# Optimization experiments

Measured on AMD Instinct MI355X. Metric: run time of the kernel, lower is better.

Reference implementation:

```python
import jax, jax.numpy as jnp
import numpy as np

N_NODES = 100000
N_EDGES = 1200000
MAX_ATOM_TYPE = 100
NUM_FEATURES = 92
GC_DIM = 64          # pre_layer_dim == gc_dim == CGConv channels
NUM_RBF = 32
NUM_GC_LAYERS = 4
CUTOFF_UPPER = 5.0
BN_EPS = 1e-5


def setup_inputs() -> dict:
    key = jax.random.key(0)
    ks = jax.random.split(key, 12)
    atom_types = jax.random.randint(ks[0], (N_NODES,), 0, MAX_ATOM_TYPE, dtype=jnp.int32)
    pos = jax.random.uniform(ks[1], (N_NODES, 3), dtype=jnp.float32) * 6.0  # box side 6 -> many dists < cutoff
    edge_index = jax.random.randint(ks[2], (2, N_EDGES), 0, N_NODES, dtype=jnp.int32)
    # parameters
    emb = jax.random.normal(ks[3], (MAX_ATOM_TYPE, NUM_FEATURES), dtype=jnp.float32)
    s = 1.0 / np.sqrt(NUM_FEATURES)
    pre_W = jax.random.uniform(ks[4], (NUM_FEATURES, GC_DIM), minval=-s, maxval=s, dtype=jnp.float32)
    pre_b = jnp.zeros((GC_DIM,), jnp.float32)
    zdim = 2 * GC_DIM + NUM_RBF  # [x_i, x_j, edge_attr]
    sz = 1.0 / np.sqrt(zdim)
    Wf = jax.random.uniform(ks[5], (NUM_GC_LAYERS, zdim, GC_DIM), minval=-sz, maxval=sz, dtype=jnp.float32)
    bf = jnp.zeros((NUM_GC_LAYERS, GC_DIM), jnp.float32)
    Ws = jax.random.uniform(ks[6], (NUM_GC_LAYERS, zdim, GC_DIM), minval=-sz, maxval=sz, dtype=jnp.float32)
    bs = jnp.zeros((NUM_GC_LAYERS, GC_DIM), jnp.float32)
    bn_gamma = jnp.ones((NUM_GC_LAYERS, GC_DIM), jnp.float32)
    bn_beta = jnp.zeros((NUM_GC_LAYERS, GC_DIM), jnp.float32)
    # ExpNormalSmearing (torchmd-net) init
    start = np.exp(-CUTOFF_UPPER)
    means = jnp.asarray(np.linspace(start, 1.0, NUM_RBF), jnp.float32)
    betas = jnp.full((NUM_RBF,), (2.0 / NUM_RBF * (1.0 - start)) ** -2, jnp.float32)
    return {"atom_types": atom_types, "pos": pos, "edge_index": edge_index,
            "emb": emb, "pre_W": pre_W, "pre_b": pre_b,
            "Wf": Wf, "bf": bf, "Ws": Ws, "bs": bs,
            "bn_gamma": bn_gamma, "bn_beta": bn_beta,
            "means": means, "betas": betas}


def _forward(atom_types, pos, edge_index, emb, pre_W, pre_b, Wf, bf, Ws, bs,
             bn_gamma, bn_beta, means, betas):
    src, dst = edge_index[0], edge_index[1]
    # distance (edge_vec = pos[src] - pos[dst])
    vec = pos[src] - pos[dst]                                  # [E,3]
    dist = jnp.sqrt(jnp.sum(vec * vec, axis=-1) + 1e-12)       # [E]
    # expnorm RBF with cosine cutoff (cutoff_lower = 0)
    cutoff = 0.5 * (jnp.cos(dist * (np.pi / CUTOFF_UPPER)) + 1.0) * (dist < CUTOFF_UPPER)
    alpha = 5.0 / CUTOFF_UPPER
    edge_attr = cutoff[:, None] * jnp.exp(
        -betas * (jnp.exp(-alpha * dist)[:, None] - means) ** 2)  # [E,NUM_RBF]
    # embedding + pre layer
    x = emb[atom_types]                                        # [N,F]
    x = jax.nn.relu(x @ pre_W + pre_b)                         # [N,C]
    # mean-aggregation degree (scatter-mean denominator)
    deg = jax.ops.segment_sum(jnp.ones_like(dist), dst, num_segments=N_NODES)
    inv_deg = jnp.where(deg > 0, 1.0 / jnp.maximum(deg, 1.0), 0.0)[:, None]
    for l in range(NUM_GC_LAYERS):
        # CGConv: z = [x_i, x_j, e]; out = x + mean_j(sigmoid(lin_f(z)) * softplus(lin_s(z)))
        z = jnp.concatenate([x[dst], x[src], edge_attr], axis=-1)   # [E, 2C+R]
        msg = jax.nn.sigmoid(z @ Wf[l] + bf[l]) * jax.nn.softplus(z @ Ws[l] + bs[l])
        agg = jax.ops.segment_sum(msg, dst, num_segments=N_NODES) * inv_deg
        x = x + agg
        # BatchNorm1d (batch statistics, biased var, as in torch training mode)
        mu = jnp.mean(x, axis=0)
        var = jnp.mean((x - mu) ** 2, axis=0)
        x = (x - mu) * jax.lax.rsqrt(var + BN_EPS) * bn_gamma[l] + bn_beta[l]
    return x


def reference(atom_types, pos, edge_index, emb, pre_W, pre_b, Wf, bf, Ws, bs,
              bn_gamma, bn_beta, means, betas):
    return _forward(atom_types, pos, edge_index, emb, pre_W, pre_b, Wf, bf, Ws, bs,
                    bn_gamma, bn_beta, means, betas)
```

## Files before the change

kernel.cpp:

```cpp
#include <hip/hip_runtime.h>
#include <math.h>

#define N_NODES 100000
#define N_EDGES 1200000
#define GC 64
#define RBF 32
#define NLAYERS 4
#define NF 92
#define NATOM 100
#define BN_EPS 1e-5f
#define TILE_GRID 2048
#define NWIN (N_EDGES / 16)
#define LOG2E 1.44269504f
#define LN2 0.69314718f

typedef _Float16 half8 __attribute__((ext_vector_type(8)));
typedef _Float16 half4 __attribute__((ext_vector_type(4)));
typedef _Float16 half2v __attribute__((ext_vector_type(2)));
typedef float f32x4 __attribute__((ext_vector_type(4)));
union U32H2 { unsigned int u; half2v h; };

__global__ __launch_bounds__(256) void deg_kernel(
    const int* __restrict__ ei, int* __restrict__ deg)
{
    int e = blockIdx.x * 256 + threadIdx.x;
    if (e >= N_EDGES) return;
    atomicAdd(&deg[ei[N_EDGES + e]], 1);
}

__global__ __launch_bounds__(256) void scan_a_kernel(const int* __restrict__ deg, int* __restrict__ bsums)
{
    __shared__ int sm[256];
    int tid = threadIdx.x;
    int i = blockIdx.x * 256 + tid;
    int v = (i < N_NODES) ? deg[i] : 0;
    sm[tid] = v;
    __syncthreads();
    for (int s = 128; s > 0; s >>= 1) {
        if (tid < s) sm[tid] += sm[tid + s];
        __syncthreads();
    }
    if (tid == 0) bsums[blockIdx.x] = sm[0];
}

__global__ __launch_bounds__(512) void scan_b_kernel(const int* __restrict__ bsums, int* __restrict__ boffs)
{
    __shared__ int sm[512];
    int tid = threadIdx.x;
    int v = (tid < 391) ? bsums[tid] : 0;
    sm[tid] = v;
    __syncthreads();
    for (int off = 1; off < 512; off <<= 1) {
        int t = (tid >= off) ? sm[tid - off] : 0;
        __syncthreads();
        sm[tid] += t;
        __syncthreads();
    }
    boffs[tid] = (tid == 0) ? 0 : sm[tid - 1];
}

__global__ __launch_bounds__(256) void scan_c_kernel(
    const int* __restrict__ deg, const int* __restrict__ boffs,
    int* __restrict__ row_st, float* __restrict__ inv_deg)
{
    __shared__ int sm[256];
    int tid = threadIdx.x;
    int i = blockIdx.x * 256 + tid;
    int v = (i < N_NODES) ? deg[i] : 0;
    sm[tid] = v;
    __syncthreads();
    for (int off = 1; off < 256; off <<= 1) {
        int t = (tid >= off) ? sm[tid - off] : 0;
        __syncthreads();
        sm[tid] += t;
        __syncthreads();
    }
    if (i <= N_NODES) row_st[i] = boffs[blockIdx.x] + sm[tid] - v;
    if (i < N_NODES) inv_deg[i] = (v > 0) ? (1.0f / (float)v) : 0.0f;
}

__global__ __launch_bounds__(256) void scatter_perm_kernel(
    const int* __restrict__ ei, const int* __restrict__ row_st,
    int* __restrict__ cursor, int* __restrict__ csr_src, int* __restrict__ csr_dst)
{
    int e = blockIdx.x * 256 + threadIdx.x;
    if (e >= N_EDGES) return;
    int s = ei[e];
    int d = ei[N_EDGES + e];
    int p = atomicAdd(&cursor[d], 1);
    int idx = row_st[d] + p;
    csr_src[idx] = s;
    csr_dst[idx] = d;
}

__global__ __launch_bounds__(256) void rbf_kernel(
    const int* __restrict__ csr_src, const int* __restrict__ csr_dst,
    const float* __restrict__ pos,
    const float* __restrict__ means, const float* __restrict__ betas,
    unsigned int* __restrict__ ea)
{
    int idx = blockIdx.x * 256 + threadIdx.x;
    if (idx >= N_EDGES) return;
    int s = csr_src[idx];
    int d = csr_dst[idx];
    float dx = pos[s * 3 + 0] - pos[d * 3 + 0];
    float dy = pos[s * 3 + 1] - pos[d * 3 + 1];
    float dz = pos[s * 3 + 2] - pos[d * 3 + 2];
    float dist = sqrtf(dx * dx + dy * dy + dz * dz + 1e-12f);

    float cut = 0.0f;
    if (dist < 5.0f) cut = 0.5f * (__cosf(dist * 0.6283185307179586f) + 1.0f);
    float ex = __expf(-dist);
    union { _Float16 h[32]; uint4 u[4]; } pk;
#pragma unroll
    for (int k = 0; k < 32; k++) {
        float v = ex - means[k];
        pk.h[k] = (_Float16)(cut * __expf(-betas[k] * v * v));
    }
    uint4* op = (uint4*)(ea + (size_t)idx * 16);
    op[0] = pk.u[0];
    op[1] = pk.u[1];
    op[2] = pk.u[2];
    op[3] = pk.u[3];
}

__global__ __launch_bounds__(256) void window_prep_kernel(
    const int* __restrict__ csr_dst, const float* __restrict__ inv_deg,
    unsigned char* __restrict__ seg8, int* __restrict__ wnode, _Float16* __restrict__ inv_e)
{
    int w = blockIdx.x * 256 + threadIdx.x;
    if (w >= NWIN) return;
    int base = w * 16;
    int prev = -1, s = -1;
    for (int k = 0; k < 16; k++) {
        int d = csr_dst[base + k];
        if (d != prev) { s++; prev = d; wnode[base + s] = d; }
        seg8[base + k] = (unsigned char)s;
        inv_e[base + k] = (_Float16)(inv_deg[d] * LN2);
    }
    for (int m = s + 1; m < 16; m++) wnode[base + m] = -1;
}

__global__ __launch_bounds__(256) void wcvt_kernel(
    const float* __restrict__ Wf, const float* __restrict__ Ws,
    _Float16* __restrict__ wf16, _Float16* __restrict__ ws16)
{
    int i = blockIdx.x * 256 + threadIdx.x;
    int l = i / (160 * GC);
    int r = i - l * 160 * GC;
    int k = r >> 6;
    int col = r & 63;
    size_t o = ((size_t)l * GC + col) * 160 + k;
    wf16[o] = (_Float16)(Wf[i] * LOG2E);
    ws16[o] = (_Float16)(Ws[i] * LOG2E);
}

__global__ __launch_bounds__(64) void atom_table_kernel(
    const float* __restrict__ emb, const float* __restrict__ pre_W,
    const float* __restrict__ pre_b, float* __restrict__ T)
{
    int a = blockIdx.x;
    int c = threadIdx.x;
    float acc = pre_b[c];
    for (int k = 0; k < NF; k++) acc = fmaf(emb[a * NF + k], pre_W[k * GC + c], acc);
    T[a * GC + c] = fmaxf(acc, 0.0f);
}

__global__ __launch_bounds__(256) void xinit_kernel(
    const int* __restrict__ atom_types, const float* __restrict__ T,
    float* __restrict__ x, _Float16* __restrict__ x16)
{
    int i = blockIdx.x * 256 + threadIdx.x;
    int n = i >> 4;
    int a = atom_types[n];
    float4 v = ((const float4*)T)[a * 16 + (i & 15)];
    ((float4*)x)[i] = v;
    half4 h = { (_Float16)v.x, (_Float16)v.y, (_Float16)v.z, (_Float16)v.w };
    ((half4*)x16)[i] = h;
}

static __device__ __forceinline__ void proj_mfma16(
    const _Float16* __restrict__ wf, const _Float16* __restrict__ ws,
    const float* __restrict__ bfv, const float* __restrict__ bsv,
    const half8 Bn[2], int cb, int node, unsigned int* __restrict__ P2u)
{
    const int lane = threadIdx.x & 63;
    const int quad = lane >> 4;
    const int r16 = lane & 15;
    f32x4 accf[2], accs[2];
#pragma unroll
    for (int sub = 0; sub < 2; sub++) {
        accf[sub] = (f32x4){0.f, 0.f, 0.f, 0.f};
        accs[sub] = (f32x4){0.f, 0.f, 0.f, 0.f};
    }
#pragma unroll
    for (int kt = 0; kt < 2; kt++) {
#pragma unroll
        for (int sub = 0; sub < 2; sub++) {
            int chan = cb + sub * 16 + r16;
            half8 a = *(const half8*)(wf + (size_t)chan * 160 + kt * 32 + quad * 8);
            half8 b = *(const half8*)(ws + (size_t)chan * 160 + kt * 32 + quad * 8);
            accf[sub] = __builtin_amdgcn_mfma_f32_16x16x32_f16(a, Bn[kt], accf[sub], 0, 0, 0);
            accs[sub] = __builtin_amdgcn_mfma_f32_16x16x32_f16(b, Bn[kt], accs[sub], 0, 0, 0);
        }
    }
#pragma unroll
    for (int sub = 0; sub < 2; sub++) {
        float4 bf4 = *(const float4*)(bfv + cb + sub * 16 + quad * 4);
        float4 bs4 = *(const float4*)(bsv + cb + sub * 16 + quad * 4);
        half8 h = { (_Float16)(accf[sub][0] + bf4.x * LOG2E), (_Float16)(accs[sub][0] + bs4.x * LOG2E),
                    (_Float16)(accf[sub][1] + bf4.y * LOG2E), (_Float16)(accs[sub][1] + bs4.y * LOG2E),
                    (_Float16)(accf[sub][2] + bf4.z * LOG2E), (_Float16)(accs[sub][2] + bs4.z * LOG2E),
                    (_Float16)(accf[sub][3] + bf4.w * LOG2E), (_Float16)(accs[sub][3] + bs4.w * LOG2E) };
        *(half8*)(P2u + (size_t)node * GC + cb + sub * 16 + quad * 4) = h;
    }
}

__global__ __launch_bounds__(256) void proj_kernel(
    const _Float16* __restrict__ x16,
    const _Float16* __restrict__ wf, const _Float16* __restrict__ ws,
    const float* __restrict__ bfv, const float* __restrict__ bsv,
    unsigned int* __restrict__ P2u)
{
    const int lane = threadIdx.x & 63;
    const int wid = threadIdx.x >> 6;
    const int quad = lane >> 4;
    const int r16 = lane & 15;
    const int wgid = blockIdx.x * 4 + wid;
    const int cb = (wgid & 1) * 32;
    const int nb = (wgid >> 1) * 16;
    half8 Bn[2];
    Bn[0] = *(const half8*)(x16 + (size_t)(nb + r16) * GC + quad * 8);
    Bn[1] = *(const half8*)(x16 + (size_t)(nb + r16) * GC + 32 + quad * 8);
    proj_mfma16(wf, ws, bfv, bsv, Bn, cb, nb + r16, P2u);
}

__global__ __launch_bounds__(256) void bnproj_kernel(
    const float* __restrict__ xn, const float* __restrict__ stats,
    const float* __restrict__ gamma, const float* __restrict__ beta,
    float* __restrict__ xout, _Float16* __restrict__ x16,
    const _Float16* __restrict__ wf, const _Float16* __restrict__ ws,
    const float* __restrict__ bfv, const float* __restrict__ bsv,
    unsigned int* __restrict__ P2u)
{
    __shared__ _Float16 lx[32 * 72];
    const int nb = blockIdx.x * 32;
    const float invN = 1.0f / (float)N_NODES;

#pragma unroll
    for (int rep = 0; rep < 2; rep++) {
        int g = rep * 256 + threadIdx.x;
        int gi = blockIdx.x * 512 + g;
        int node = g >> 4;
        int c4 = (g & 15) * 4;
        float4 v = ((const float4*)xn)[gi];
        float vv[4] = {v.x, v.y, v.z, v.w};
        float o[4];
#pragma unroll
        for (int t = 0; t < 4; t++) {
            int c = c4 + t;
            float mu = stats[c] * invN;
            float var = stats[64 + c] * invN - mu * mu;
            float sc = gamma[c] * rsqrtf(var + BN_EPS);
            o[t] = (vv[t] - mu) * sc + beta[c];
        }
        ((float4*)xout)[gi] = make_float4(o[0], o[1], o[2], o[3]);
        half4 h = { (_Float16)o[0], (_Float16)o[1], (_Float16)o[2], (_Float16)o[3] };
        ((half4*)x16)[gi] = h;
        *(half4*)(lx + node * 72 + c4) = h;
    }
    __syncthreads();

    const int lane = threadIdx.x & 63;
    const int wid = threadIdx.x >> 6;
    const int quad = lane >> 4;
    const int r16 = lane & 15;
    const int cb = (wid & 1) * 32;
    const int tn = (wid >> 1) * 16 + r16;
    half8 Bn[2];
    Bn[0] = *(const half8*)(lx + tn * 72 + quad * 8);
    Bn[1] = *(const half8*)(lx + tn * 72 + 32 + quad * 8);
    proj_mfma16(wf, ws, bfv, bsv, Bn, cb, nb + tn, P2u);
}

static __device__ __forceinline__ void compute_win(
    half8 S0, half8 S1, half8 E,
    const unsigned int (&pv)[8], unsigned int segq, int4 wn4, half4 inv4,
    const half8 (&WGF)[3][2], const half8 (&WGS)[3][2],
    int r16, int quad, int cb, float* __restrict__ x)
{
    f32x4 accf[2], accs[2];
#pragma unroll
    for (int ctl = 0; ctl < 2; ctl++) {
#pragma unroll
        for (int rr = 0; rr < 4; rr++) {
            U32H2 t; t.u = pv[ctl * 4 + rr];
            accf[ctl][rr] = (float)t.h.x;
            accs[ctl][rr] = (float)t.h.y;
        }
    }
    __builtin_amdgcn_s_setprio(1);
#pragma unroll
    for (int ctl = 0; ctl < 2; ctl++) {
        accf[ctl] = __builtin_amdgcn_mfma_f32_16x16x32_f16(S0, WGF[0][ctl], accf[ctl], 0, 0, 0);
        accs[ctl] = __builtin_amdgcn_mfma_f32_16x16x32_f16(S0, WGS[0][ctl], accs[ctl], 0, 0, 0);
        accf[ctl] = __builtin_amdgcn_mfma_f32_16x16x32_f16(S1, WGF[1][ctl], accf[ctl], 0, 0, 0);
        accs[ctl] = __builtin_amdgcn_mfma_f32_16x16x32_f16(S1, WGS[1][ctl], accs[ctl], 0, 0, 0);
        accf[ctl] = __builtin_amdgcn_mfma_f32_16x16x32_f16(E,  WGF[2][ctl], accf[ctl], 0, 0, 0);
        accs[ctl] = __builtin_amdgcn_mfma_f32_16x16x32_f16(E,  WGS[2][ctl], accs[ctl], 0, 0, 0);
    }
    __builtin_amdgcn_s_setprio(0);
    half4 msgh[2];
#pragma unroll
    for (int ctl = 0; ctl < 2; ctl++) {
#pragma unroll
        for (int rr = 0; rr < 4; rr++) {
            float af = accf[ctl][rr];
            float as = accs[ctl][rr];
            float sg = __builtin_amdgcn_rcpf(1.0f + __builtin_amdgcn_exp2f(-af));
            float sp = __builtin_amdgcn_logf(1.0f + __builtin_amdgcn_exp2f(as));
            msgh[ctl][rr] = (_Float16)(sg * sp);
        }
    }
    half4 am;
#pragma unroll
    for (int j = 0; j < 4; j++) {
        int sj = (segq >> (8 * j)) & 0xff;
        am[j] = (sj == r16) ? inv4[j] : (_Float16)0.0f;
    }
    int wa[4] = { wn4.x, wn4.y, wn4.z, wn4.w };
    const f32x4 zf = (f32x4){0.0f, 0.0f, 0.0f, 0.0f};
#pragma unroll
    for (int ctl = 0; ctl < 2; ctl++) {
        f32x4 red = __builtin_amdgcn_mfma_f32_16x16x16f16(am, msgh[ctl], zf, 0, 0, 0);
#pragma unroll
        for (int rr = 0; rr < 4; rr++) {
            int nd = wa[rr];
            if (nd >= 0) atomicAdd(&x[(size_t)nd * GC + cb + ctl * 16 + r16], red[rr]);
        }
    }
}

#define LOADSET(S0_, S1_, EE_, SGQ_, WN4_, INV4_, PV_, SRC_, D4_, WW_)               \
    S0_ = *(const half8*)(x16 + (size_t)(SRC_) * GC + quad * 8);                     \
    S1_ = *(const half8*)(x16 + (size_t)(SRC_) * GC + 32 + quad * 8);                \
    EE_ = *(const half8*)(ea + ((size_t)(WW_) * 16 + r16) * RBF + quad * 8);         \
    SGQ_ = *(const unsigned int*)(seg8 + (WW_) * 16 + quad * 4);                     \
    WN4_ = *(const int4*)(wnode + (WW_) * 16 + quad * 4);                            \
    INV4_ = *(const half4*)(inv_e + (WW_) * 16 + quad * 4);                          \
    {                                                                                 \
        int dd0 = (D4_).x, dd1 = (D4_).y, dd2 = (D4_).z, dd3 = (D4_).w;              \
        PV_[0] = P2u[(size_t)dd0 * GC + cb + r16];                                   \
        PV_[1] = P2u[(size_t)dd1 * GC + cb + r16];                                   \
        PV_[2] = P2u[(size_t)dd2 * GC + cb + r16];                                   \
        PV_[3] = P2u[(size_t)dd3 * GC + cb + r16];                                   \
        PV_[4] = P2u[(size_t)dd0 * GC + cb + 16 + r16];                              \
        PV_[5] = P2u[(size_t)dd1 * GC + cb + 16 + r16];                              \
        PV_[6] = P2u[(size_t)dd2 * GC + cb + 16 + r16];                              \
        PV_[7] = P2u[(size_t)dd3 * GC + cb + 16 + r16];                              \
    }

__global__ __launch_bounds__(256, 3) void win_mfma_kernel(
    const _Float16* __restrict__ x16, const _Float16* __restrict__ ea,
    const int* __restrict__ csr_src, const int* __restrict__ csr_dst,
    const unsigned char* __restrict__ seg8, const int* __restrict__ wnode,
    const _Float16* __restrict__ inv_e, const unsigned int* __restrict__ P2u,
    const _Float16* __restrict__ wf16, const _Float16* __restrict__ ws16,
    float* __restrict__ x)
{
    const int lane = threadIdx.x & 63;
    const int wid = __builtin_amdgcn_readfirstlane(threadIdx.x >> 6);
    const int quad = lane >> 4;
    const int r16 = lane & 15;
    const int wgid = blockIdx.x * 4 + wid;
    const int cb = (wgid & 1) * 32;
    int w = wgid >> 1;
    const int NSEQ = TILE_GRID * 2;

    half8 WGF[3][2], WGS[3][2];
#pragma unroll
    for (int ctl = 0; ctl < 2; ctl++) {
        const _Float16* wfp = wf16 + (size_t)(cb + ctl * 16 + r16) * 160 + 64 + quad * 8;
        const _Float16* wsp = ws16 + (size_t)(cb + ctl * 16 + r16) * 160 + 64 + quad * 8;
#pragma unroll
        for (int kt = 0; kt < 3; kt++) {
            WGF[kt][ctl] = *(const half8*)(wfp + kt * 32);
            WGS[kt][ctl] = *(const half8*)(wsp + kt * 32);
        }
    }

    int sA = csr_src[w * 16 + r16];
    int4 d4A = *(const int4*)(csr_dst + w * 16 + quad * 4);
    half8 AS0, AS1, AE;
    unsigned int apv[8], asgq;
    int4 awn4;
    half4 ainv4;
    LOADSET(AS0, AS1, AE, asgq, awn4, ainv4, apv, sA, d4A, w);

    int wB = w + NSEQ; if (wB >= NWIN) wB = NWIN - 1;
    int sB = csr_src[wB * 16 + r16];
    int4 d4B = *(const int4*)(csr_dst + wB * 16 + quad * 4);
    half8 BS0, BS1, BE;
    unsigned int bpv[8], bsgq;
    int4 bwn4;
    half4 binv4;
    LOADSET(BS0, BS1, BE, bsgq, bwn4, binv4, bpv, sB, d4B, wB);

    int wC = wB + NSEQ; if (wC >= NWIN) wC = NWIN - 1;
    int sC = csr_src[wC * 16 + r16];
    int4 d4C = *(const int4*)(csr_dst + wC * 16 + quad * 4);

    while (true) {
        compute_win(AS0, AS1, AE, apv, asgq, awn4, ainv4,
                    WGF, WGS, r16, quad, cb, x);
        LOADSET(AS0, AS1, AE, asgq, awn4, ainv4, apv, sC, d4C, wC);
        wC += NSEQ; if (wC >= NWIN) wC = NWIN - 1;
        sC = csr_src[wC * 16 + r16];
        d4C = *(const int4*)(csr_dst + wC * 16 + quad * 4);
        w += NSEQ;
        if (w >= NWIN) break;

        compute_win(BS0, BS1, BE, bpv, bsgq, bwn4, binv4,
                    WGF, WGS, r16, quad, cb, x);
        LOADSET(BS0, BS1, BE, bsgq, bwn4, binv4, bpv, sC, d4C, wC);
        wC += NSEQ; if (wC >= NWIN) wC = NWIN - 1;
        sC = csr_src[wC * 16 + r16];
        d4C = *(const int4*)(csr_dst + wC * 16 + quad * 4);
        w += NSEQ;
        if (w >= NWIN) break;
    }
}

__global__ __launch_bounds__(256) void stats_kernel(const float* __restrict__ x, float* __restrict__ stats)
{
    const int lane = threadIdx.x & 63;
    const int wid = threadIdx.x >> 6;
    int w = blockIdx.x * 4 + wid;
    float s1 = 0.0f, s2 = 0.0f;
    for (int n = w; n < N_NODES; n += 1024) {
        float v = x[(size_t)n * GC + lane];
        s1 += v;
        s2 = fmaf(v, v, s2);
    }
    __shared__ float rs1[4][64];
    __shared__ float rs2[4][64];
    rs1[wid][lane] = s1;
    rs2[wid][lane] = s2;
    __syncthreads();
    if (threadIdx.x < 64) {
        atomicAdd(&stats[lane], rs1[0][lane] + rs1[1][lane] + rs1[2][lane] + rs1[3][lane]);
    } else if (threadIdx.x < 128) {
        int c = threadIdx.x & 63;
        atomicAdd(&stats[64 + c], rs2[0][c] + rs2[1][c] + rs2[2][c] + rs2[3][c]);
    }
}

__global__ __launch_bounds__(256) void bn_kernel(
    const float* __restrict__ xn, const float* __restrict__ stats,
    const float* __restrict__ gamma, const float* __restrict__ beta,
    float* __restrict__ out)
{
    int i = blockIdx.x * 256 + threadIdx.x;
    int c4 = (i & 15) * 4;
    float4 v = ((const float4*)xn)[i];
    float vv[4] = {v.x, v.y, v.z, v.w};
    float o[4];
    const float invN = 1.0f / (float)N_NODES;
#pragma unroll
    for (int t = 0; t < 4; t++) {
        int c = c4 + t;
        float mu = stats[c] * invN;
        float var = stats[64 + c] * invN - mu * mu;
        float sc = gamma[c] * rsqrtf(var + BN_EPS);
        o[t] = (vv[t] - mu) * sc + beta[c];
    }
    ((float4*)out)[i] = make_float4(o[0], o[1], o[2], o[3]);
}

extern "C" void kernel_launch(void* const* d_in, const int* in_sizes, int n_in,
                              void* d_out, int out_size, void* d_ws, size_t ws_size,
                              hipStream_t stream)
{
    const int* atom_types = (const int*)d_in[0];
    const float* pos = (const float*)d_in[1];
    const int* edge_index = (const int*)d_in[2];
    const float* emb = (const float*)d_in[3];
    const float* pre_W = (const float*)d_in[4];
    const float* pre_b = (const float*)d_in[5];
    const float* Wf = (const float*)d_in[6];
    const float* bf = (const float*)d_in[7];
    const float* Ws = (const float*)d_in[8];
    const float* bs = (const float*)d_in[9];
    const float* gamma = (const float*)d_in[10];
    const float* beta = (const float*)d_in[11];
    const float* means = (const float*)d_in[12];
    const float* betas = (const float*)d_in[13];

    char* base = (char*)d_ws;
    char* p = base;
    auto alloc = [&](size_t bytes) -> char* {
        char* r = p;
        p += (bytes + 255) & ~(size_t)255;
        return r;
    };
    unsigned int* ea = (unsigned int*)alloc((size_t)N_EDGES * RBF * 2);
    float* x = (float*)alloc((size_t)N_NODES * GC * 4);
    _Float16* x16 = (_Float16*)alloc((size_t)N_NODES * GC * 2);
    unsigned int* P2u = (unsigned int*)alloc((size_t)N_NODES * GC * 4);
    int* csr_src = (int*)alloc((size_t)N_EDGES * 4);
    int* csr_dst = (int*)alloc((size_t)N_EDGES * 4);
    int* wnode = (int*)alloc((size_t)N_EDGES * 4);
    unsigned char* seg8 = (unsigned char*)alloc((size_t)N_EDGES);
    _Float16* inv_e = (_Float16*)alloc((size_t)N_EDGES * 2);
    _Float16* wf16 = (_Float16*)alloc((size_t)NLAYERS * GC * 160 * 2);
    _Float16* ws16 = (_Float16*)alloc((size_t)NLAYERS * GC * 160 * 2);
    int* row_st = (int*)alloc((size_t)(N_NODES + 1) * 4);
    float* inv_deg = (float*)alloc((size_t)N_NODES * 4);
    float* T = (float*)alloc((size_t)NATOM * GC * 4);
    int* bsums = (int*)alloc(512 * 4);
    int* boffs = (int*)alloc(512 * 4);
    const size_t ZR_INTS = (size_t)2 * N_NODES + 128 * NLAYERS + 64;
    char* zr = alloc(ZR_INTS * 4);
    int* deg = (int*)zr;
    int* cursor = deg + N_NODES;
    float* stats = (float*)(cursor + N_NODES);

    if ((size_t)(p - base) > ws_size) return;

    (void)hipMemsetAsync(zr, 0, ZR_INTS * 4, stream);

    const int EG = (N_EDGES + 255) / 256;
    deg_kernel<<<EG, 256, 0, stream>>>(edge_index, deg);
    scan_a_kernel<<<391, 256, 0, stream>>>(deg, bsums);
    scan_b_kernel<<<1, 512, 0, stream>>>(bsums, boffs);
    scan_c_kernel<<<391, 256, 0, stream>>>(deg, boffs, row_st, inv_deg);
    scatter_perm_kernel<<<EG, 256, 0, stream>>>(edge_index, row_st, cursor, csr_src, csr_dst);
    rbf_kernel<<<EG, 256, 0, stream>>>(csr_src, csr_dst, pos, means, betas, ea);
    window_prep_kernel<<<(NWIN + 255) / 256, 256, 0, stream>>>(csr_dst, inv_deg, seg8, wnode, inv_e);
    wcvt_kernel<<<(NLAYERS * 160 * GC) / 256, 256, 0, stream>>>(Wf, Ws, wf16, ws16);
    atom_table_kernel<<<NATOM, 64, 0, stream>>>(emb, pre_W, pre_b, T);
    xinit_kernel<<<N_NODES * 16 / 256, 256, 0, stream>>>(atom_types, T, x, x16);
    proj_kernel<<<N_NODES / 32, 256, 0, stream>>>(x16, wf16, ws16, bf, bs, P2u);

    for (int l = 0; l < NLAYERS; l++) {
        win_mfma_kernel<<<TILE_GRID, 256, 0, stream>>>(
            x16, (const _Float16*)ea, csr_src, csr_dst, seg8, wnode, inv_e, P2u,
            wf16 + (size_t)l * GC * 160, ws16 + (size_t)l * GC * 160, x);
        stats_kernel<<<256, 256, 0, stream>>>(x, stats + l * 128);
        if (l < NLAYERS - 1) {
            bnproj_kernel<<<N_NODES / 32, 256, 0, stream>>>(
                x, stats + l * 128, gamma + l * GC, beta + l * GC, x, x16,
                wf16 + (size_t)(l + 1) * GC * 160, ws16 + (size_t)(l + 1) * GC * 160,
                bf + (l + 1) * GC, bs + (l + 1) * GC, P2u);
        } else {
            bn_kernel<<<N_NODES * 16 / 256, 256, 0, stream>>>(
                x, stats + l * 128, gamma + l * GC, beta + l * GC, (float*)d_out);
        }
    }
}
```

Before: 854.6 us.

## Defer per-window P2/segment loads into compute and raise occupancy to four blocks

The per-window P2u projection gathers, segment bytes, window node indices and inverse degrees are no longer prefetched into registers for the double-buffered windows. They are loaded inside compute_win and the projection is added after the MFMAs instead of seeding the accumulators. This frees registers so launch bounds can go from 3 to 4 blocks per CU, at the cost of exposing those gather latencies within each window. Separately, scatter_perm now writes one int2 (src,dst) pair per edge into the ea buffer and a new split kernel unpacks it into csr_src and csr_dst.

```diff
diff --git a/kernel.cpp b/kernel.cpp
--- a/kernel.cpp
+++ b/kernel.cpp
@@ -81,16 +81,24 @@
 
 __global__ __launch_bounds__(256) void scatter_perm_kernel(
     const int* __restrict__ ei, const int* __restrict__ row_st,
-    int* __restrict__ cursor, int* __restrict__ csr_src, int* __restrict__ csr_dst)
+    int* __restrict__ cursor, int2* __restrict__ csr_sd)
 {
     int e = blockIdx.x * 256 + threadIdx.x;
     if (e >= N_EDGES) return;
     int s = ei[e];
     int d = ei[N_EDGES + e];
     int p = atomicAdd(&cursor[d], 1);
-    int idx = row_st[d] + p;
-    csr_src[idx] = s;
-    csr_dst[idx] = d;
+    csr_sd[row_st[d] + p] = make_int2(s, d);
+}
+
+__global__ __launch_bounds__(256) void split_kernel(
+    const int2* __restrict__ csr_sd, int* __restrict__ csr_src, int* __restrict__ csr_dst)
+{
+    int i = blockIdx.x * 256 + threadIdx.x;
+    if (i >= N_EDGES) return;
+    int2 v = csr_sd[i];
+    csr_src[i] = v.x;
+    csr_dst[i] = v.y;
 }
 
 __global__ __launch_bounds__(256) void rbf_kernel(
@@ -284,39 +292,51 @@
 }
 
 static __device__ __forceinline__ void compute_win(
-    half8 S0, half8 S1, half8 E,
-    const unsigned int (&pv)[8], unsigned int segq, int4 wn4, half4 inv4,
+    half8 S0, half8 S1, half8 E, int4 d4, int moff,
     const half8 (&WGF)[3][2], const half8 (&WGS)[3][2],
-    int r16, int quad, int cb, float* __restrict__ x)
-{
+    int r16, int quad, int cb,
+    const unsigned char* __restrict__ seg8, const int* __restrict__ wnode,
+    const _Float16* __restrict__ inv_e, const unsigned int* __restrict__ P2u,
+    float* __restrict__ x)
+{
+    unsigned int pv0, pv1, pv2, pv3, pv4, pv5, pv6, pv7;
+    {
+        const unsigned int* p0 = P2u + (size_t)d4.x * GC + cb + r16;
+        const unsigned int* p1 = P2u + (size_t)d4.y * GC + cb + r16;
+        const unsigned int* p2 = P2u + (size_t)d4.z * GC + cb + r16;
+        const unsigned int* p3 = P2u + (size_t)d4.w * GC + cb + r16;
+        pv0 = p0[0];  pv4 = p0[16];
+        pv1 = p1[0];  pv5 = p1[16];
+        pv2 = p2[0];  pv6 = p2[16];
+        pv3 = p3[0];  pv7 = p3[16];
+    }
+    unsigned int segq = *(const unsigned int*)(seg8 + moff + quad * 4);
+    int4 wn4 = *(const int4*)(wnode + moff + quad * 4);
+    half4 inv4 = *(const half4*)(inv_e + moff + quad * 4);
+
+    const f32x4 zf = (f32x4){0.0f, 0.0f, 0.0f, 0.0f};
     f32x4 accf[2], accs[2];
+    __builtin_amdgcn_s_setprio(1);
 #pragma unroll
     for (int ctl = 0; ctl < 2; ctl++) {
-#pragma unroll
-        for (int rr = 0; rr < 4; rr++) {
-            U32H2 t; t.u = pv[ctl * 4 + rr];
-            accf[ctl][rr] = (float)t.h.x;
-            accs[ctl][rr] = (float)t.h.y;
-        }
-    }
-    __builtin_amdgcn_s_setprio(1);
-#pragma unroll
-    for (int ctl = 0; ctl < 2; ctl++) {
-        accf[ctl] = __builtin_amdgcn_mfma_f32_16x16x32_f16(S0, WGF[0][ctl], accf[ctl], 0, 0, 0);
-        accs[ctl] = __builtin_amdgcn_mfma_f32_16x16x32_f16(S0, WGS[0][ctl], accs[ctl], 0, 0, 0);
+        accf[ctl] = __builtin_amdgcn_mfma_f32_16x16x32_f16(S0, WGF[0][ctl], zf, 0, 0, 0);
+        accs[ctl] = __builtin_amdgcn_mfma_f32_16x16x32_f16(S0, WGS[0][ctl], zf, 0, 0, 0);
         accf[ctl] = __builtin_amdgcn_mfma_f32_16x16x32_f16(S1, WGF[1][ctl], accf[ctl], 0, 0, 0);
         accs[ctl] = __builtin_amdgcn_mfma_f32_16x16x32_f16(S1, WGS[1][ctl], accs[ctl], 0, 0, 0);
         accf[ctl] = __builtin_amdgcn_mfma_f32_16x16x32_f16(E,  WGF[2][ctl], accf[ctl], 0, 0, 0);
         accs[ctl] = __builtin_amdgcn_mfma_f32_16x16x32_f16(E,  WGS[2][ctl], accs[ctl], 0, 0, 0);
     }
     __builtin_amdgcn_s_setprio(0);
+
+    unsigned int pvv[8] = {pv0, pv1, pv2, pv3, pv4, pv5, pv6, pv7};
     half4 msgh[2];
 #pragma unroll
     for (int ctl = 0; ctl < 2; ctl++) {
 #pragma unroll
         for (int rr = 0; rr < 4; rr++) {
-            float af = accf[ctl][rr];
-            float as = accs[ctl][rr];
+            U32H2 t; t.u = pvv[ctl * 4 + rr];
+            float af = accf[ctl][rr] + (float)t.h.x;
+            float as = accs[ctl][rr] + (float)t.h.y;
             float sg = __builtin_amdgcn_rcpf(1.0f + __builtin_amdgcn_exp2f(-af));
             float sp = __builtin_amdgcn_logf(1.0f + __builtin_amdgcn_exp2f(as));
             msgh[ctl][rr] = (_Float16)(sg * sp);
@@ -329,7 +349,6 @@
         am[j] = (sj == r16) ? inv4[j] : (_Float16)0.0f;
     }
     int wa[4] = { wn4.x, wn4.y, wn4.z, wn4.w };
-    const f32x4 zf = (f32x4){0.0f, 0.0f, 0.0f, 0.0f};
 #pragma unroll
     for (int ctl = 0; ctl < 2; ctl++) {
         f32x4 red = __builtin_amdgcn_mfma_f32_16x16x16f16(am, msgh[ctl], zf, 0, 0, 0);
@@ -341,26 +360,12 @@
     }
 }
 
-#define LOADSET(S0_, S1_, EE_, SGQ_, WN4_, INV4_, PV_, SRC_, D4_, WW_)               \
+#define LOADSET(S0_, S1_, EE_, SRC_, WW_)                                            \
     S0_ = *(const half8*)(x16 + (size_t)(SRC_) * GC + quad * 8);                     \
     S1_ = *(const half8*)(x16 + (size_t)(SRC_) * GC + 32 + quad * 8);                \
-    EE_ = *(const half8*)(ea + ((size_t)(WW_) * 16 + r16) * RBF + quad * 8);         \
-    SGQ_ = *(const unsigned int*)(seg8 + (WW_) * 16 + quad * 4);                     \
-    WN4_ = *(const int4*)(wnode + (WW_) * 16 + quad * 4);                            \
-    INV4_ = *(const half4*)(inv_e + (WW_) * 16 + quad * 4);                          \
-    {                                                                                 \
-        int dd0 = (D4_).x, dd1 = (D4_).y, dd2 = (D4_).z, dd3 = (D4_).w;              \
-        PV_[0] = P2u[(size_t)dd0 * GC + cb + r16];                                   \
-        PV_[1] = P2u[(size_t)dd1 * GC + cb + r16];                                   \
-        PV_[2] = P2u[(size_t)dd2 * GC + cb + r16];                                   \
-        PV_[3] = P2u[(size_t)dd3 * GC + cb + r16];                                   \
-        PV_[4] = P2u[(size_t)dd0 * GC + cb + 16 + r16];                              \
-        PV_[5] = P2u[(size_t)dd1 * GC + cb + 16 + r16];                              \
-        PV_[6] = P2u[(size_t)dd2 * GC + cb + 16 + r16];                              \
-        PV_[7] = P2u[(size_t)dd3 * GC + cb + 16 + r16];                              \
-    }
-
-__global__ __launch_bounds__(256, 3) void win_mfma_kernel(
+    EE_ = *(const half8*)(ea + ((size_t)(WW_) * 16 + r16) * RBF + quad * 8);
+
+__global__ __launch_bounds__(256, 4) void win_mfma_kernel(
     const _Float16* __restrict__ x16, const _Float16* __restrict__ ea,
     const int* __restrict__ csr_src, const int* __restrict__ csr_dst,
     const unsigned char* __restrict__ seg8, const int* __restrict__ wnode,
@@ -392,37 +397,35 @@
     int sA = csr_src[w * 16 + r16];
     int4 d4A = *(const int4*)(csr_dst + w * 16 + quad * 4);
     half8 AS0, AS1, AE;
-    unsigned int apv[8], asgq;
-    int4 awn4;
-    half4 ainv4;
-    LOADSET(AS0, AS1, AE, asgq, awn4, ainv4, apv, sA, d4A, w);
+    LOADSET(AS0, AS1, AE, sA, w);
+    int moffA = w * 16;
 
     int wB = w + NSEQ; if (wB >= NWIN) wB = NWIN - 1;
     int sB = csr_src[wB * 16 + r16];
     int4 d4B = *(const int4*)(csr_dst + wB * 16 + quad * 4);
     half8 BS0, BS1, BE;
-    unsigned int bpv[8], bsgq;
-    int4 bwn4;
-    half4 binv4;
-    LOADSET(BS0, BS1, BE, bsgq, bwn4, binv4, bpv, sB, d4B, wB);
+    LOADSET(BS0, BS1, BE, sB, wB);
+    int moffB = wB * 16;
 
     int wC = wB + NSEQ; if (wC >= NWIN) wC = NWIN - 1;
     int sC = csr_src[wC * 16 + r16];
     int4 d4C = *(const int4*)(csr_dst + wC * 16 + quad * 4);
 
     while (true) {
-        compute_win(AS0, AS1, AE, apv, asgq, awn4, ainv4,
-                    WGF, WGS, r16, quad, cb, x);
-        LOADSET(AS0, AS1, AE, asgq, awn4, ainv4, apv, sC, d4C, wC);
+        compute_win(AS0, AS1, AE, d4A, moffA,
+                    WGF, WGS, r16, quad, cb, seg8, wnode, inv_e, P2u, x);
+        LOADSET(AS0, AS1, AE, sC, wC);
+        d4A = d4C; moffA = wC * 16;
         wC += NSEQ; if (wC >= NWIN) wC = NWIN - 1;
         sC = csr_src[wC * 16 + r16];
         d4C = *(const int4*)(csr_dst + wC * 16 + quad * 4);
         w += NSEQ;
         if (w >= NWIN) break;
 
-        compute_win(BS0, BS1, BE, bpv, bsgq, bwn4, binv4,
-                    WGF, WGS, r16, quad, cb, x);
-        LOADSET(BS0, BS1, BE, bsgq, bwn4, binv4, bpv, sC, d4C, wC);
+        compute_win(BS0, BS1, BE, d4B, moffB,
+                    WGF, WGS, r16, quad, cb, seg8, wnode, inv_e, P2u, x);
+        LOADSET(BS0, BS1, BE, sC, wC);
+        d4B = d4C; moffB = wC * 16;
         wC += NSEQ; if (wC >= NWIN) wC = NWIN - 1;
         sC = csr_src[wC * 16 + r16];
         d4C = *(const int4*)(csr_dst + wC * 16 + quad * 4);
@@ -525,6 +528,8 @@
     int* cursor = deg + N_NODES;
     float* stats = (float*)(cursor + N_NODES);
 
+    int2* csr_sd = (int2*)ea;
+
     if ((size_t)(p - base) > ws_size) return;
 
     (void)hipMemsetAsync(zr, 0, ZR_INTS * 4, stream);
@@ -534,7 +539,8 @@
     scan_a_kernel<<<391, 256, 0, stream>>>(deg, bsums);
     scan_b_kernel<<<1, 512, 0, stream>>>(bsums, boffs);
     scan_c_kernel<<<391, 256, 0, stream>>>(deg, boffs, row_st, inv_deg);
-    scatter_perm_kernel<<<EG, 256, 0, stream>>>(edge_index, row_st, cursor, csr_src, csr_dst);
+    scatter_perm_kernel<<<EG, 256, 0, stream>>>(edge_index, row_st, cursor, csr_sd);
+    split_kernel<<<EG, 256, 0, stream>>>(csr_sd, csr_src, csr_dst);
     rbf_kernel<<<EG, 256, 0, stream>>>(csr_src, csr_dst, pos, means, betas, ea);
     window_prep_kernel<<<(NWIN + 255) / 256, 256, 0, stream>>>(csr_dst, inv_deg, seg8, wnode, inv_e);
     wcvt_kernel<<<(NLAYERS * 160 * GC) / 256, 256, 0, stream>>>(Wf, Ws, wf16, ws16);
```

Result: slower. 891.2 us (+4.3%).
